# Kernel tuning notes

Measured on AMD Instinct MI355X. Metric: run time of the kernel, lower is better.

## Reference

```python
import jax, jax.numpy as jnp
import numpy as np


def _unfold(x, k):
    # x: [B, C, H, W] -> [B, C, S, L] with S=k*k (row-major patch order), L=H*W
    B, C, H, W = x.shape
    pad = k // 2
    xp = jnp.pad(x, ((0, 0), (0, 0), (pad, pad), (pad, pad)))
    patches = jnp.stack(
        [xp[:, :, r:r + H, c:c + W] for r in range(k) for c in range(k)], axis=2
    )  # [B, C, S, H, W]
    return patches.reshape(B, C, k * k, H * W)


def setup_inputs() -> dict:
    key = jax.random.key(0)
    ks = jax.random.split(key, 8)
    B, C, H, W = 8, 64, 128, 128
    R, Cout = 4, 128
    x = jax.random.normal(ks[0], (B, C, H, W), dtype=jnp.float32)
    gate_w = jax.random.normal(ks[1], (R, C), dtype=jnp.float32) * 0.05   # 1x1 gate conv weight
    gate_b = jax.random.normal(ks[2], (R,), dtype=jnp.float32) * 0.01
    theta = jax.random.normal(ks[3], (R,), dtype=jnp.float32) * 0.5       # learned directions
    raw_sigma_u = jax.random.normal(ks[4], (R,), dtype=jnp.float32) * 0.1
    raw_sigma_s = jax.random.normal(ks[5], (R,), dtype=jnp.float32) * 0.1
    pw_w = jax.random.normal(ks[6], (Cout, R * C), dtype=jnp.float32) * (1.0 / np.sqrt(R * C).astype(np.float32))
    pw_b = jax.random.normal(ks[7], (Cout,), dtype=jnp.float32) * 0.01
    return {"x": x, "gate_w": gate_w, "gate_b": gate_b, "theta": theta,
            "raw_sigma_u": raw_sigma_u, "raw_sigma_s": raw_sigma_s,
            "pw_w": pw_w, "pw_b": pw_b}


def reference(x, gate_w, gate_b, theta, raw_sigma_u, raw_sigma_s, pw_w, pw_b):
    k = 3
    B, C, H, W = x.shape
    R = theta.shape[0]
    S, L = k * k, H * W

    x_un = _unfold(x, k)                                         # [B, C, S, L]

    # 1x1 gate conv + fuzzy softmax over rules
    logits = jnp.einsum('bchw,rc->brhw', x, gate_w) + gate_b[None, :, None, None]
    mu = jax.nn.softmax(logits, axis=1)                          # [B, R, H, W]
    mu_un = _unfold(mu, k)                                       # [B, R, S, L]
    s_center = (k // 2) * k + (k // 2)
    mu_center = mu_un[:, :, s_center:s_center + 1, :]            # [B, R, 1, L]

    # anisotropic Gaussian kernel per rule over integer offsets (row-major)
    grid = np.arange(k, dtype=np.float32) - k // 2
    dy = jnp.asarray(np.repeat(grid, k))                         # [S]
    dx = jnp.asarray(np.tile(grid, k))                           # [S]
    cos_t, sin_t = jnp.cos(theta)[:, None], jnp.sin(theta)[:, None]
    proj_u = cos_t * dx[None, :] + sin_t * dy[None, :]           # [R, S]
    proj_s = -sin_t * dx[None, :] + cos_t * dy[None, :]
    su = (jax.nn.softplus(raw_sigma_u) + 1e-4)[:, None]
    ss = (jax.nn.softplus(raw_sigma_s) + 1e-4)[:, None]
    kern = jnp.exp(-proj_u ** 2 / su ** 2 - proj_s ** 2 / ss ** 2)  # [R, S]

    alpha = mu_center * mu_un * kern[None, :, :, None]           # [B, R, S, L]
    alpha_sum = jnp.maximum(alpha.sum(axis=(1, 2), keepdims=True), 1e-8)
    alpha = alpha / alpha_sum

    agg = jnp.einsum('brsl,bcsl->brcl', alpha, x_un)             # [B, R, C, L]
    agg_flat = agg.reshape(B, R * C, L)
    out = jnp.einsum('bnl,on->bol', agg_flat, pw_w) + pw_b[None, :, None]
    return out.reshape(B, -1, H, W)
```

## Files before the change

kernel.cpp:

```cpp
#include <hip/hip_runtime.h>
#include <math.h>

#define CC 64
#define RR 4
#define HH 128
#define WW 128
#define BB 8
#define COUT 128
#define XST 72
#define ALS 44

typedef __attribute__((ext_vector_type(8))) short short8;
typedef __attribute__((ext_vector_type(4))) float f32x4;
typedef __attribute__((ext_vector_type(2))) float f32x2;

__device__ __forceinline__ unsigned short f2bf(float f) {
  unsigned u = __float_as_uint(f);
  u += 0x7fffu + ((u >> 16) & 1u);
  return (unsigned short)(u >> 16);
}
__device__ __forceinline__ float bf2f(unsigned short h) {
  return __uint_as_float(((unsigned)h) << 16);
}
__device__ __forceinline__ float blo(unsigned u) { return __uint_as_float(u << 16); }
__device__ __forceinline__ float bhi(unsigned u) { return __uint_as_float(u & 0xffff0000u); }

__global__ __launch_bounds__(256) void k_pre(const float* __restrict__ theta,
                                             const float* __restrict__ rsu,
                                             const float* __restrict__ rss,
                                             const float* __restrict__ pw,
                                             const float* __restrict__ gw,
                                             float* __restrict__ wkern,
                                             unsigned short* __restrict__ pwb,
                                             unsigned short* __restrict__ gwb) {
  int i = blockIdx.x * 256 + threadIdx.x;
  if (i < COUT * RR * CC) pwb[i] = f2bf(pw[i]);
  if (blockIdx.x == 0 && threadIdx.x < RR * 9) {
    int t = threadIdx.x;
    int r = t / 9, s = t % 9;
    float dy = (float)(s / 3 - 1), dx = (float)(s % 3 - 1);
    float ct = cosf(theta[r]), st = sinf(theta[r]);
    float su = log1pf(expf(rsu[r])) + 1e-4f;
    float sv = log1pf(expf(rss[r])) + 1e-4f;
    float pu = ct * dx + st * dy;
    float ps = -st * dx + ct * dy;
    wkern[t] = expf(-(pu * pu) / (su * su) - (ps * ps) / (sv * sv));
  }
  if (blockIdx.x == 1) {
    #pragma unroll
    for (int k = 0; k < 4; ++k) {
      int j = k * 256 + threadIdx.x;
      gwb[j] = (j < RR * CC) ? f2bf(gw[j]) : (unsigned short)0;
    }
  }
}

__global__ __launch_bounds__(256, 3) void k_fused(const float* __restrict__ x,
                                                  const float* __restrict__ gb,
                                                  const float* __restrict__ wkern,
                                                  const unsigned short* __restrict__ pwb,
                                                  const unsigned short* __restrict__ gwb,
                                                  const float* __restrict__ pb,
                                                  float* __restrict__ out) {
  __shared__ unsigned short xsT[160][XST];
  __shared__ float mus[RR][4][40];
  __shared__ unsigned short alp[64][ALS];
  __shared__ float rsum[RR][64];
  __shared__ __align__(16) unsigned short aggs[32][264];

  int tid = threadIdx.x;
  int raw = blockIdx.x;
  int bid = (raw & 7) * 256 + (raw >> 3);
  int b = bid >> 8;
  int rem = bid & 255;
  int h0 = (rem >> 2) << 1;
  int w0 = (rem & 3) << 5;

  int lane = tid & 63;
  int wv = tid >> 6;
  int lr = lane & 15, lq = lane >> 4;
  int o0 = wv << 5;

  short8 a0r[8], a1r[8];
  {
    const unsigned short* pA = pwb + ((o0 + lr) << 8) + (lq << 3);
    #pragma unroll
    for (int ks = 0; ks < 8; ++ks) {
      a0r[ks] = *(const short8*)(pA + (ks << 5));
      a1r[ks] = *(const short8*)(pA + 4096 + (ks << 5));
    }
  }
  short8 am0 = *(const short8*)(gwb + (lr << 6) + (lq << 3));
  short8 am1 = *(const short8*)(gwb + (lr << 6) + 32 + (lq << 3));
  float4 pbv0 = *(const float4*)&pb[o0 + (lq << 2)];
  float4 pbv1 = *(const float4*)&pb[o0 + 16 + (lq << 2)];
  float gb0 = gb[0], gb1 = gb[1], gb2 = gb[2], gb3 = gb[3];

  #pragma unroll
  for (int k = 0; k < 10; ++k) {
    unsigned idx = (unsigned)(k * 256 + tid);
    unsigned c4 = idx % 10u;
    unsigned pair = idx / 10u;
    int c = pair >> 2, row = pair & 3;
    int gcol = w0 - 4 + (c4 << 2);
    int grow = h0 - 1 + row;
    float4 v = make_float4(0.f, 0.f, 0.f, 0.f);
    if ((unsigned)gcol < WW && (unsigned)grow < HH)
      v = *(const float4*)(x + (((size_t)b * CC + c) << 14) + (grow << 7) + gcol);
    int sp = row * 40 + (c4 << 2);
    xsT[sp][c]     = f2bf(v.x);
    xsT[sp + 1][c] = f2bf(v.y);
    xsT[sp + 2][c] = f2bf(v.z);
    xsT[sp + 3][c] = f2bf(v.w);
  }
  __syncthreads();

  for (int j = wv; j < 9; j += 4) {
    int p = (j << 4) + lr;
    int pcl = p > 135 ? 135 : p;
    unsigned y = (unsigned)pcl / 34u;
    int cxo = pcl - (int)(y * 34u);
    int pos = (int)y * 40 + 3 + cxo;
    short8 b0 = *(const short8*)&xsT[pos][lq << 3];
    short8 b1 = *(const short8*)&xsT[pos][32 + (lq << 3)];
    f32x4 mac = (f32x4){0.f, 0.f, 0.f, 0.f};
    mac = __builtin_amdgcn_mfma_f32_16x16x32_bf16(am0, b0, mac, 0, 0, 0);
    mac = __builtin_amdgcn_mfma_f32_16x16x32_bf16(am1, b1, mac, 0, 0, 0);
    if (lq == 0 && p < 136) {
      int grow = h0 - 1 + (int)y, gcol = w0 - 1 + cxo;
      float lg0 = mac[0] + gb0, lg1 = mac[1] + gb1;
      float lg2 = mac[2] + gb2, lg3 = mac[3] + gb3;
      float m = fmaxf(fmaxf(lg0, lg1), fmaxf(lg2, lg3));
      float e0 = expf(lg0 - m), e1 = expf(lg1 - m);
      float e2 = expf(lg2 - m), e3 = expf(lg3 - m);
      float inv = 1.0f / (e0 + e1 + e2 + e3);
      if (!((unsigned)grow < HH && (unsigned)gcol < WW)) inv = 0.0f;
      mus[0][y][3 + cxo] = e0 * inv;
      mus[1][y][3 + cxo] = e1 * inv;
      mus[2][y][3 + cxo] = e2 * inv;
      mus[3][y][3 + cxo] = e3 * inv;
    }
  }
  __syncthreads();

  {
    int t = tid & 63, r = tid >> 6;
    int prow = t >> 5, pcol = t & 31;
    float mc = mus[r][prow + 1][pcol + 4];
    float sum = 0.f;
    #pragma unroll
    for (int s = 0; s < 9; ++s) {
      float av = mc * mus[r][prow + s / 3][pcol + 3 + s % 3] * wkern[r * 9 + s];
      alp[t][(s << 2) + r] = f2bf(av);
      sum += av;
    }
    rsum[r][t] = sum;
  }
  __syncthreads();

  #pragma unroll
  for (int p = 0; p < 2; ++p) {
    {
      int t = tid & 31, cg = tid >> 5, c0 = cg << 3;
      int px = (p << 5) + t;
      float inv = 1.0f / fmaxf(rsum[0][px] + rsum[1][px] + rsum[2][px] + rsum[3][px], 1e-8f);

      uint2 ad[9];
      #pragma unroll
      for (int s = 0; s < 9; ++s) ad[s] = *(const uint2*)(&alp[px][s << 2]);

      f32x2 cacc[4][4];
      #pragma unroll
      for (int r = 0; r < 4; ++r)
        #pragma unroll
        for (int j = 0; j < 4; ++j) cacc[r][j] = (f32x2){0.f, 0.f};

      #pragma unroll
      for (int s = 0; s < 9; ++s) {
        uint4 ux = *(const uint4*)&xsT[(p + s / 3) * 40 + t + 3 + s % 3][c0];
        f32x2 xv0 = {blo(ux.x), bhi(ux.x)};
        f32x2 xv1 = {blo(ux.y), bhi(ux.y)};
        f32x2 xv2 = {blo(ux.z), bhi(ux.z)};
        f32x2 xv3 = {blo(ux.w), bhi(ux.w)};
        unsigned adx = ad[s].x, ady = ad[s].y;
        float af0 = blo(adx), af1 = bhi(adx), af2 = blo(ady), af3 = bhi(ady);
        f32x2 A0 = {af0, af0}, A1 = {af1, af1}, A2 = {af2, af2}, A3 = {af3, af3};
        cacc[0][0] += A0 * xv0; cacc[0][1] += A0 * xv1; cacc[0][2] += A0 * xv2; cacc[0][3] += A0 * xv3;
        cacc[1][0] += A1 * xv0; cacc[1][1] += A1 * xv1; cacc[1][2] += A1 * xv2; cacc[1][3] += A1 * xv3;
        cacc[2][0] += A2 * xv0; cacc[2][1] += A2 * xv1; cacc[2][2] += A2 * xv2; cacc[2][3] += A2 * xv3;
        cacc[3][0] += A3 * xv0; cacc[3][1] += A3 * xv1; cacc[3][2] += A3 * xv2; cacc[3][3] += A3 * xv3;
      }
      #pragma unroll
      for (int r = 0; r < 4; ++r) {
        short8 wvv;
        #pragma unroll
        for (int j = 0; j < 4; ++j) {
          wvv[2 * j]     = (short)f2bf(cacc[r][j][0] * inv);
          wvv[2 * j + 1] = (short)f2bf(cacc[r][j][1] * inv);
        }
        *(short8*)&aggs[t][(r << 6) + c0] = wvv;
      }
    }
    __syncthreads();

    f32x4 dacc[2][2];
    #pragma unroll
    for (int i = 0; i < 2; ++i)
      #pragma unroll
      for (int j = 0; j < 2; ++j) dacc[i][j] = (f32x4){0.f, 0.f, 0.f, 0.f};

    #pragma unroll
    for (int ks = 0; ks < 8; ++ks) {
      short8 b0 = *(const short8*)&aggs[lr][(ks << 5) + (lq << 3)];
      short8 b1 = *(const short8*)&aggs[16 + lr][(ks << 5) + (lq << 3)];
      dacc[0][0] = __builtin_amdgcn_mfma_f32_16x16x32_bf16(a0r[ks], b0, dacc[0][0], 0, 0, 0);
      dacc[0][1] = __builtin_amdgcn_mfma_f32_16x16x32_bf16(a0r[ks], b1, dacc[0][1], 0, 0, 0);
      dacc[1][0] = __builtin_amdgcn_mfma_f32_16x16x32_bf16(a1r[ks], b0, dacc[1][0], 0, 0, 0);
      dacc[1][1] = __builtin_amdgcn_mfma_f32_16x16x32_bf16(a1r[ks], b1, dacc[1][1], 0, 0, 0);
    }

    #pragma unroll
    for (int oi = 0; oi < 2; ++oi) {
      float4 pbv = oi ? pbv1 : pbv0;
      #pragma unroll
      for (int q = 0; q < 4; ++q) {
        int o = o0 + (oi << 4) + (lq << 2) + q;
        size_t base = (((size_t)b * COUT + o) << 14) + ((h0 + p) << 7) + w0;
        out[base + lr]      = dacc[oi][0][q] + pbv[q];
        out[base + 16 + lr] = dacc[oi][1][q] + pbv[q];
      }
    }
    if (p == 0) __syncthreads();
  }
}

extern "C" void kernel_launch(void* const* d_in, const int* in_sizes, int n_in,
                              void* d_out, int out_size, void* d_ws, size_t ws_size,
                              hipStream_t stream) {
  const float* x     = (const float*)d_in[0];
  const float* gw    = (const float*)d_in[1];
  const float* gb    = (const float*)d_in[2];
  const float* theta = (const float*)d_in[3];
  const float* rsu   = (const float*)d_in[4];
  const float* rss   = (const float*)d_in[5];
  const float* pw    = (const float*)d_in[6];
  const float* pb    = (const float*)d_in[7];
  float* outp = (float*)d_out;

  float* wkern = (float*)d_ws;
  unsigned short* pwb = (unsigned short*)(wkern + 64);
  unsigned short* gwb = pwb + COUT * RR * CC;

  k_pre<<<128, 256, 0, stream>>>(theta, rsu, rss, pw, gw, wkern, pwb, gwb);
  k_fused<<<BB * (HH / 2) * (WW / 32), 256, 0, stream>>>(x, gb, wkern, pwb, gwb, pb, outp);
}
```

Before: 59.26 us.

## Swizzle LDS tiles and load four channels per thread for packed stores

Applies XOR swizzles to the channel-block index of the shared x tile and the aggregation buffer, and updates every reader and writer to match, to cut LDS bank conflicts. The global-to-LDS staging loop now has each thread load four channels' float4 values and write a packed ushort4 per spatial position, replacing the previous four scattered 2-byte stores. This cuts the number of LDS store instructions and issues more global loads per thread, at the cost of extra index arithmetic and some redundant conversions left in the staging code.

```diff
diff --git a/kernel.cpp b/kernel.cpp
--- a/kernel.cpp
+++ b/kernel.cpp
@@ -19,11 +19,10 @@
   u += 0x7fffu + ((u >> 16) & 1u);
   return (unsigned short)(u >> 16);
 }
-__device__ __forceinline__ float bf2f(unsigned short h) {
-  return __uint_as_float(((unsigned)h) << 16);
-}
 __device__ __forceinline__ float blo(unsigned u) { return __uint_as_float(u << 16); }
 __device__ __forceinline__ float bhi(unsigned u) { return __uint_as_float(u & 0xffff0000u); }
+__device__ __forceinline__ int swzx(int cb, int sp) { return cb ^ ((sp >> 3) & 7); }
+__device__ __forceinline__ int swza(int cb, int row) { return cb ^ ((row >> 3) & 3); }
 
 __global__ __launch_bounds__(256) void k_pre(const float* __restrict__ theta,
                                              const float* __restrict__ rsu,
@@ -97,21 +96,36 @@
   float gb0 = gb[0], gb1 = gb[1], gb2 = gb[2], gb3 = gb[3];
 
   #pragma unroll
-  for (int k = 0; k < 10; ++k) {
-    unsigned idx = (unsigned)(k * 256 + tid);
-    unsigned c4 = idx % 10u;
-    unsigned pair = idx / 10u;
-    int c = pair >> 2, row = pair & 3;
-    int gcol = w0 - 4 + (c4 << 2);
-    int grow = h0 - 1 + row;
-    float4 v = make_float4(0.f, 0.f, 0.f, 0.f);
-    if ((unsigned)gcol < WW && (unsigned)grow < HH)
-      v = *(const float4*)(x + (((size_t)b * CC + c) << 14) + (grow << 7) + gcol);
-    int sp = row * 40 + (c4 << 2);
-    xsT[sp][c]     = f2bf(v.x);
-    xsT[sp + 1][c] = f2bf(v.y);
-    xsT[sp + 2][c] = f2bf(v.z);
-    xsT[sp + 3][c] = f2bf(v.w);
+  for (int k = 0; k < 3; ++k) {
+    int item = k * 256 + tid;
+    if (item < 640) {
+      int c4 = item % 10;
+      int rest = item / 10;
+      int row = rest & 3, cquad = rest >> 2;
+      int c = cquad << 2;
+      int gcol = w0 - 4 + (c4 << 2);
+      int grow = h0 - 1 + row;
+      float4 v0 = make_float4(0.f,0.f,0.f,0.f), v1 = v0, v2 = v0, v3 = v0;
+      if ((unsigned)gcol < WW && (unsigned)grow < HH) {
+        const float* xp = x + (((size_t)b * CC + c) << 14) + (grow << 7) + gcol;
+        v0 = *(const float4*)xp;
+        v1 = *(const float4*)(xp + (1 << 14));
+        v2 = *(const float4*)(xp + (2 << 14));
+        v3 = *(const float4*)(xp + (3 << 14));
+      }
+      int spb = row * 40 + (c4 << 2);
+      int cb = cquad >> 1, sub = (cquad & 1) << 2;
+      float4 vv[4] = {v0, v1, v2, v3};
+      #pragma unroll
+      for (int j = 0; j < 4; ++j) {
+        int sp = spb + j;
+        ushort4 uv;
+        uv.x = f2bf(vv[0].x); uv.y = f2bf(vv[1].x); uv.z = f2bf(vv[2].x); uv.w = f2bf(vv[3].x);
+        float f0 = (&vv[0].x)[j], f1 = (&vv[1].x)[j], f2v = (&vv[2].x)[j], f3 = (&vv[3].x)[j];
+        uv.x = f2bf(f0); uv.y = f2bf(f1); uv.z = f2bf(f2v); uv.w = f2bf(f3);
+        *(ushort4*)&xsT[sp][(swzx(cb, sp) << 3) + sub] = uv;
+      }
+    }
   }
   __syncthreads();
 
@@ -121,8 +135,8 @@
     unsigned y = (unsigned)pcl / 34u;
     int cxo = pcl - (int)(y * 34u);
     int pos = (int)y * 40 + 3 + cxo;
-    short8 b0 = *(const short8*)&xsT[pos][lq << 3];
-    short8 b1 = *(const short8*)&xsT[pos][32 + (lq << 3)];
+    short8 b0 = *(const short8*)&xsT[pos][swzx(lq, pos) << 3];
+    short8 b1 = *(const short8*)&xsT[pos][swzx(4 + lq, pos) << 3];
     f32x4 mac = (f32x4){0.f, 0.f, 0.f, 0.f};
     mac = __builtin_amdgcn_mfma_f32_16x16x32_bf16(am0, b0, mac, 0, 0, 0);
     mac = __builtin_amdgcn_mfma_f32_16x16x32_bf16(am1, b1, mac, 0, 0, 0);
@@ -161,7 +175,7 @@
   #pragma unroll
   for (int p = 0; p < 2; ++p) {
     {
-      int t = tid & 31, cg = tid >> 5, c0 = cg << 3;
+      int t = tid & 31, cg = tid >> 5;
       int px = (p << 5) + t;
       float inv = 1.0f / fmaxf(rsum[0][px] + rsum[1][px] + rsum[2][px] + rsum[3][px], 1e-8f);
 
@@ -177,7 +191,8 @@
 
       #pragma unroll
       for (int s = 0; s < 9; ++s) {
-        uint4 ux = *(const uint4*)&xsT[(p + s / 3) * 40 + t + 3 + s % 3][c0];
+        int sp = (p + s / 3) * 40 + t + 3 + s % 3;
+        uint4 ux = *(const uint4*)&xsT[sp][swzx(cg, sp) << 3];
         f32x2 xv0 = {blo(ux.x), bhi(ux.x)};
         f32x2 xv1 = {blo(ux.y), bhi(ux.y)};
         f32x2 xv2 = {blo(ux.z), bhi(ux.z)};
@@ -198,7 +213,7 @@
           wvv[2 * j]     = (short)f2bf(cacc[r][j][0] * inv);
           wvv[2 * j + 1] = (short)f2bf(cacc[r][j][1] * inv);
         }
-        *(short8*)&aggs[t][(r << 6) + c0] = wvv;
+        *(short8*)&aggs[t][swza((r << 3) + cg, t) << 3] = wvv;
       }
     }
     __syncthreads();
@@ -211,8 +226,8 @@
 
     #pragma unroll
     for (int ks = 0; ks < 8; ++ks) {
-      short8 b0 = *(const short8*)&aggs[lr][(ks << 5) + (lq << 3)];
-      short8 b1 = *(const short8*)&aggs[16 + lr][(ks << 5) + (lq << 3)];
+      short8 b0 = *(const short8*)&aggs[lr][swza((ks << 2) + lq, lr) << 3];
+      short8 b1 = *(const short8*)&aggs[16 + lr][swza((ks << 2) + lq, 16 + lr) << 3];
       dacc[0][0] = __builtin_amdgcn_mfma_f32_16x16x32_bf16(a0r[ks], b0, dacc[0][0], 0, 0, 0);
       dacc[0][1] = __builtin_amdgcn_mfma_f32_16x16x32_bf16(a0r[ks], b1, dacc[0][1], 0, 0, 0);
       dacc[1][0] = __builtin_amdgcn_mfma_f32_16x16x32_bf16(a1r[ks], b0, dacc[1][0], 0, 0, 0);
```

Result: faster. 51.10 us (-13.8%).
